# Performance work log

Hardware: AMD Instinct MI355X
Metric: run time of the kernel (lower is better)

Reference implementation:

```python
import jax, jax.numpy as jnp
import numpy as np

H, KV, D = 16, 4, 128
WIN = 512
EPS = 1e-6


def rms_norm(x, w):
    # x: [..., D]
    return x * jax.lax.rsqrt(jnp.mean(x * x, axis=-1, keepdims=True) + EPS) * w


def rotate_half(x):
    x1, x2 = jnp.split(x, 2, axis=-1)
    return jnp.concatenate([-x2, x1], axis=-1)


def setup_inputs() -> dict:
    key = jax.random.key(0)
    ks = jax.random.split(key, 8)
    B, L, hidden = 2, 2048, 2048
    x = jax.random.normal(ks[0], (B, L, hidden), jnp.float32)
    # realistic RoPE tables
    inv_freq = 1.0 / (10000.0 ** (np.arange(0, D, 2, dtype=np.float32) / D))
    t = np.arange(L, dtype=np.float32)
    freqs = np.outer(t, inv_freq)  # [L, D/2]
    emb = np.concatenate([freqs, freqs], axis=-1)  # [L, D]
    cos = jnp.asarray(np.cos(emb), jnp.float32)
    sin = jnp.asarray(np.sin(emb), jnp.float32)
    s = 0.02
    Wq = jax.random.normal(ks[1], (H * D, hidden), jnp.float32) * s
    Wk = jax.random.normal(ks[2], (KV * D, hidden), jnp.float32) * s
    Wv = jax.random.normal(ks[3], (KV * D, hidden), jnp.float32) * s
    Wo = jax.random.normal(ks[4], (hidden, H * D), jnp.float32) * s
    q_norm_w = jnp.ones((D,), jnp.float32)
    k_norm_w = jnp.ones((D,), jnp.float32)
    return {"x": x, "cos": cos, "sin": sin, "Wq": Wq, "Wk": Wk, "Wv": Wv,
            "Wo": Wo, "q_norm_w": q_norm_w, "k_norm_w": k_norm_w}


def reference(x, cos, sin, Wq, Wk, Wv, Wo, q_norm_w, k_norm_w):
    B, L, _ = x.shape
    # projections (torch Linear: y = x @ W.T)
    q = (x @ Wq.T).reshape(B, L, H, D)
    k = (x @ Wk.T).reshape(B, L, KV, D)
    v = (x @ Wv.T).reshape(B, L, KV, D)
    # QK RMSNorm, then [B, heads, L, D]
    q = jnp.transpose(rms_norm(q, q_norm_w), (0, 2, 1, 3))
    k = jnp.transpose(rms_norm(k, k_norm_w), (0, 2, 1, 3))
    v = jnp.transpose(v, (0, 2, 1, 3))
    # RoPE
    c = cos[None, None]  # [1,1,L,D]
    s = sin[None, None]
    q = q * c + rotate_half(q) * s
    k = k * c + rotate_half(k) * s
    # GQA repeat_interleave over head dim
    n_rep = H // KV
    k = jnp.repeat(k, n_rep, axis=1)
    v = jnp.repeat(v, n_rep, axis=1)
    # sliding-window additive bias [L, L]
    idx = jnp.arange(L)
    in_win = jnp.abs(idx[:, None] - idx[None, :]) <= WIN
    bias = jnp.where(in_win, 0.0, jnp.finfo(x.dtype).min).astype(x.dtype)
    # SDPA
    scale = 1.0 / jnp.sqrt(jnp.asarray(D, x.dtype))
    scores = jnp.einsum('bhqd,bhkd->bhqk', q, k) * scale + bias[None, None]
    attn = jax.nn.softmax(scores, axis=-1)
    out = jnp.einsum('bhqk,bhkd->bhqd', attn, v)  # [B,H,L,D]
    out = jnp.transpose(out, (0, 2, 1, 3)).reshape(B, L, H * D)
    return out @ Wo.T
```

## Files before the change

### kernel.cpp

```cpp
#include <hip/hip_runtime.h>
#include <hip/hip_bf16.h>


typedef unsigned short u16;
typedef unsigned int u32;
typedef __attribute__((ext_vector_type(8))) short bf16x8;
typedef __attribute__((ext_vector_type(4))) float f32x4;

#define AS1 __attribute__((address_space(1)))
#define AS3 __attribute__((address_space(3)))

__device__ __forceinline__ u16 f2b(float f) {
  union { float f; u32 u; } c; c.f = f;
  return (u16)((c.u + 0x8000u) >> 16);
}
__device__ __forceinline__ float b2f(u16 u) {
  union { u32 u; float f; } c; c.u = ((u32)u) << 16; return c.f;
}

__global__ __launch_bounds__(256) void cvt_all(const float* __restrict__ x,
                                               const float* __restrict__ wq,
                                               const float* __restrict__ wk,
                                               const float* __restrict__ wv,
                                               const float* __restrict__ wo,
                                               u16* __restrict__ xb,
                                               u16* __restrict__ wqkvb,
                                               u16* __restrict__ wob) {
  int blk = blockIdx.x;
  const float* s; u16* d; int off;
  if (blk < 8192)       { s = x;  d = xb;              off = blk * 1024; }
  else if (blk < 12288) { s = wq; d = wqkvb;           off = (blk - 8192) * 1024; }
  else if (blk < 13312) { s = wk; d = wqkvb + 4194304; off = (blk - 12288) * 1024; }
  else if (blk < 14336) { s = wv; d = wqkvb + 5242880; off = (blk - 13312) * 1024; }
  else                  { s = wo; d = wob;             off = (blk - 14336) * 1024; }
  int i = off + threadIdx.x * 4;
  float4 v = *(const float4*)(s + i);
  ushort4 o;
  o.x = f2b(v.x); o.y = f2b(v.y); o.z = f2b(v.z); o.w = f2b(v.w);
  *(ushort4*)(d + i) = o;
}

__global__ __launch_bounds__(256) void gemm_qkv(const u16* __restrict__ A,
                                                const u16* __restrict__ Bm,
                                                const float* __restrict__ cosT,
                                                const float* __restrict__ sinT,
                                                const float* __restrict__ qw,
                                                const float* __restrict__ kw,
                                                u16* __restrict__ qo,
                                                u16* __restrict__ ko,
                                                u16* __restrict__ vt) {
  constexpr int K = 2048;
  __shared__ u16 As[128][64];
  __shared__ u16 Bs[128][64];
  __shared__ float Rs[2][2][64];
  const int tid  = threadIdx.x;
  const int w    = tid >> 6, lane = tid & 63, quad = lane >> 4, l16 = lane & 15;
  const int wm   = w >> 1, wn = w & 1;
  const int m0   = blockIdx.y * 128;
  const int hh   = blockIdx.x;

  f32x4 zero = {0.f, 0.f, 0.f, 0.f};
  f32x4 acc[4][4];
#pragma unroll
  for (int i = 0; i < 4; i++)
#pragma unroll
    for (int j = 0; j < 4; j++) acc[i][j] = zero;

  const int srow = lane >> 3;
  const int swz8 = ((lane & 7) ^ (lane >> 3)) * 8;
  const int n0   = hh * 128;

  for (int k0 = 0; k0 < K; k0 += 64) {
#pragma unroll
    for (int p = 0; p < 4; ++p) {
      int row = p * 32 + w * 8 + srow;
      __builtin_amdgcn_global_load_lds(
          (const AS1 void*)(A + (size_t)(m0 + row) * K + k0 + swz8),
          (AS3 void*)((char*)&As[0][0] + p * 4096 + w * 1024), 16, 0, 0);
      __builtin_amdgcn_global_load_lds(
          (const AS1 void*)(Bm + (size_t)(n0 + row) * K + k0 + swz8),
          (AS3 void*)((char*)&Bs[0][0] + p * 4096 + w * 1024), 16, 0, 0);
    }
    __syncthreads();
#pragma unroll
    for (int kk = 0; kk < 64; kk += 32) {
      const int cs = ((kk >> 3) + quad) ^ (l16 & 7);
      bf16x8 af[4], bfr[4];
#pragma unroll
      for (int i = 0; i < 4; i++)
        af[i] = *(const bf16x8*)((const char*)&As[0][0] +
                                 (wm * 64 + i * 16 + l16) * 128 + cs * 16);
#pragma unroll
      for (int j = 0; j < 4; j++)
        bfr[j] = *(const bf16x8*)((const char*)&Bs[0][0] +
                                  (wn * 32 + (j & 1) * 16 + (j >> 1) * 64 + l16) * 128 + cs * 16);
#pragma unroll
      for (int i = 0; i < 4; i++)
#pragma unroll
        for (int j = 0; j < 4; j++)
          acc[i][j] = __builtin_amdgcn_mfma_f32_16x16x32_bf16(af[i], bfr[j], acc[i][j], 0, 0, 0);
    }
    __syncthreads();
  }

  const int bidx = m0 >> 11;
  const int lbase = (m0 & 2047) + wm * 64;

  if (hh < 20) {
    float ssq[4][4];
#pragma unroll
    for (int i = 0; i < 4; i++)
#pragma unroll
      for (int r = 0; r < 4; r++) {
        float s2 = acc[i][0][r] * acc[i][0][r] + acc[i][1][r] * acc[i][1][r] +
                   acc[i][2][r] * acc[i][2][r] + acc[i][3][r] * acc[i][3][r];
#pragma unroll
        for (int m = 1; m < 16; m <<= 1) s2 += __shfl_xor(s2, m, 64);
        ssq[i][r] = s2;
      }
    if (l16 == 0) {
#pragma unroll
      for (int i = 0; i < 4; i++)
#pragma unroll
        for (int r = 0; r < 4; r++)
          Rs[wm][wn][i * 16 + quad * 4 + r] = ssq[i][r];
    }
    __syncthreads();

    float inv[4][4];
#pragma unroll
    for (int i = 0; i < 4; i++)
#pragma unroll
      for (int r = 0; r < 4; r++) {
        int row64 = i * 16 + quad * 4 + r;
        float sum = Rs[wm][0][row64] + Rs[wm][1][row64];
        inv[i][r] = rsqrtf(sum * (1.0f / 128.0f) + 1e-6f);
      }

    const float* wt = hh < 16 ? qw : kw;
    const float qs_ = hh < 16 ? 0.08838834764831845f * 1.4426950408889634f : 1.0f;
    u16* dst; size_t hb;
    if (hh < 16) { dst = qo; hb = (size_t)(bidx * 16 + hh) * 2048 * 128; }
    else         { dst = ko; hb = (size_t)(bidx * 4 + (hh - 16)) * 2048 * 128; }

#pragma unroll
    for (int j = 0; j < 2; ++j) {
      const int d = wn * 32 + j * 16 + l16;
      const float wtd = wt[d], wtdp = wt[d + 64];
#pragma unroll
      for (int i = 0; i < 4; i++) {
#pragma unroll
        for (int r = 0; r < 4; r++) {
          int l = lbase + i * 16 + quad * 4 + r;
          float nv0 = acc[i][j][r]     * inv[i][r] * wtd;
          float nv1 = acc[i][j + 2][r] * inv[i][r] * wtdp;
          float c0 = cosT[l * 128 + d],      s0v = sinT[l * 128 + d];
          float c1 = cosT[l * 128 + d + 64], s1v = sinT[l * 128 + d + 64];
          float o0 = (nv0 * c0 - nv1 * s0v) * qs_;
          float o1 = (nv1 * c1 + nv0 * s1v) * qs_;
          dst[hb + (size_t)l * 128 + d]      = f2b(o0);
          dst[hb + (size_t)l * 128 + d + 64] = f2b(o1);
        }
      }
    }
  } else {
    const int kv = hh - 20;
    u16* dv = vt + (size_t)(bidx * 4 + kv) * 128 * 2048;
#pragma unroll
    for (int i = 0; i < 4; i++) {
      int l0 = lbase + i * 16 + quad * 4;
#pragma unroll
      for (int j = 0; j < 4; j++) {
        int d = wn * 32 + (j & 1) * 16 + (j >> 1) * 64 + l16;
        u16 p[4];
#pragma unroll
        for (int r = 0; r < 4; r++) p[r] = f2b(acc[i][j][r]);
        *(uint2*)(dv + (size_t)d * 2048 + l0) = *(uint2*)p;
      }
    }
  }
}

__global__ __launch_bounds__(256) void gemm_bt(const u16* __restrict__ A,
                                               const u16* __restrict__ Bm,
                                               float* __restrict__ C,
                                               int M, int N, int K) {
  __shared__ u16 As[128][64];
  __shared__ u16 Bs[128][64];
  const int tid  = threadIdx.x;
  const int w    = tid >> 6, lane = tid & 63, quad = lane >> 4, l16 = lane & 15;
  const int wm   = w >> 1, wn = w & 1;
  const int m0   = blockIdx.y * 128, n0 = blockIdx.x * 128;

  f32x4 zero = {0.f, 0.f, 0.f, 0.f};
  f32x4 acc[4][4];
#pragma unroll
  for (int i = 0; i < 4; i++)
#pragma unroll
    for (int j = 0; j < 4; j++) acc[i][j] = zero;

  const int srow = lane >> 3;
  const int swz8 = ((lane & 7) ^ (lane >> 3)) * 8;

  for (int k0 = 0; k0 < K; k0 += 64) {
#pragma unroll
    for (int p = 0; p < 4; ++p) {
      int row = p * 32 + w * 8 + srow;
      __builtin_amdgcn_global_load_lds(
          (const AS1 void*)(A + (size_t)(m0 + row) * K + k0 + swz8),
          (AS3 void*)((char*)&As[0][0] + p * 4096 + w * 1024), 16, 0, 0);
      __builtin_amdgcn_global_load_lds(
          (const AS1 void*)(Bm + (size_t)(n0 + row) * K + k0 + swz8),
          (AS3 void*)((char*)&Bs[0][0] + p * 4096 + w * 1024), 16, 0, 0);
    }
    __syncthreads();
#pragma unroll
    for (int kk = 0; kk < 64; kk += 32) {
      const int cs = ((kk >> 3) + quad) ^ (l16 & 7);
      bf16x8 af[4], bfr[4];
#pragma unroll
      for (int i = 0; i < 4; i++)
        af[i] = *(const bf16x8*)((const char*)&As[0][0] +
                                 (wm * 64 + i * 16 + l16) * 128 + cs * 16);
#pragma unroll
      for (int j = 0; j < 4; j++)
        bfr[j] = *(const bf16x8*)((const char*)&Bs[0][0] +
                                  (wn * 64 + j * 16 + l16) * 128 + cs * 16);
#pragma unroll
      for (int i = 0; i < 4; i++)
#pragma unroll
        for (int j = 0; j < 4; j++)
          acc[i][j] = __builtin_amdgcn_mfma_f32_16x16x32_bf16(af[i], bfr[j], acc[i][j], 0, 0, 0);
    }
    __syncthreads();
  }

#pragma unroll
  for (int i = 0; i < 4; i++) {
#pragma unroll
    for (int r = 0; r < 4; r++) {
      int gr = m0 + wm * 64 + i * 16 + quad * 4 + r;
#pragma unroll
      for (int j = 0; j < 4; j++) {
        int gc = n0 + wn * 64 + j * 16 + l16;
        C[(size_t)gr * N + gc] = acc[i][j][r];
      }
    }
  }
}

__global__ __launch_bounds__(512) void flash_swa(const u16* __restrict__ Q,
                                                 const u16* __restrict__ Kg,
                                                 const u16* __restrict__ VTg,
                                                 u16* __restrict__ Og) {
  constexpr int L = 2048, D = 128;
  __shared__ u16 Ks[2][64][128];
  __shared__ u16 Vt[2][128][64];
  __shared__ u16 Ps[8][32][72];

  const int flat = blockIdx.x;
  const int kvh  = flat & 3;
  const int b    = (flat >> 2) & 1;
  const int q0   = (flat >> 3) * 64;
  const int tid = threadIdx.x;
  const int w = tid >> 6, lane = tid & 63, quad = lane >> 4, l16 = lane & 15;
  const int hd = kvh * 4 + (w >> 1);
  const int qh = w & 1;

  const u16* Qb  = Q   + (size_t)(b * 16 + hd)  * L * D;
  const u16* Kb  = Kg  + (size_t)(b * 4 + kvh) * L * D;
  const u16* VTb = VTg + (size_t)(b * 4 + kvh) * D * L;

  bf16x8 qf[2][4];
#pragma unroll
  for (int qs = 0; qs < 2; ++qs) {
    int qr = q0 + qh * 32 + qs * 16 + l16;
#pragma unroll
    for (int ks = 0; ks < 4; ++ks)
      qf[qs][ks] = *(const bf16x8*)(Qb + (size_t)qr * D + ks * 32 + quad * 8);
  }
  const int qi0 = q0 + qh * 32 + l16;

  int kt0   = q0 > 512 ? q0 - 512 : 0;
  int ktend = q0 + 64 + 512; if (ktend > L) ktend = L;
  const int nt = (ktend - kt0) >> 6;

  const u16* srcK[2];
  const u16* srcV[2];
#pragma unroll
  for (int j = 0; j < 2; ++j) {
    int rk = w * 8 + j * 4 + quad;
    int ck = ((lane & 15) ^ (rk & 7)) * 8;
    srcK[j] = Kb + (size_t)(kt0 + rk) * D + ck;
    int rv = w * 16 + j * 8 + (lane >> 3);
    int cv = ((lane & 7) ^ ((lane >> 3) & 7)) * 8;
    srcV[j] = VTb + (size_t)rv * L + kt0 + cv;
  }

#define STAGE(bb) do {                                                        \
    char* kdst = (char*)&Ks[bb][0][0] + w * 2048;                             \
    char* vdst = (char*)&Vt[bb][0][0] + w * 2048;                             \
    _Pragma("unroll")                                                         \
    for (int j = 0; j < 2; ++j) {                                             \
      __builtin_amdgcn_global_load_lds((const AS1 void*)srcK[j],              \
          (AS3 void*)(kdst + j * 1024), 16, 0, 0);                            \
      srcK[j] += 64 * D;                                                      \
    }                                                                         \
    _Pragma("unroll")                                                         \
    for (int j = 0; j < 2; ++j) {                                             \
      __builtin_amdgcn_global_load_lds((const AS1 void*)srcV[j],              \
          (AS3 void*)(vdst + j * 1024), 16, 0, 0);                            \
      srcV[j] += 64;                                                          \
    }                                                                         \
  } while (0)

  f32x4 zero = {0.f, 0.f, 0.f, 0.f};
  f32x4 o[2][8];
#pragma unroll
  for (int qs = 0; qs < 2; ++qs)
#pragma unroll
    for (int i = 0; i < 8; i++) o[qs][i] = zero;
  float lrow[2] = {0.f, 0.f};

  STAGE(0);
  __syncthreads();
  int cur = 0;

  for (int t = 0; t < nt; ++t) {
    const int kt = kt0 + t * 64;
    if (t + 1 < nt) STAGE(cur ^ 1);

    const char* kbase = (const char*)&Ks[cur][0][0];
    const char* vbase = (const char*)&Vt[cur][0][0];

    f32x4 s[2][4];
#pragma unroll
    for (int qs = 0; qs < 2; ++qs)
#pragma unroll
      for (int ct = 0; ct < 4; ct++) s[qs][ct] = zero;
    __builtin_amdgcn_s_setprio(1);
#pragma unroll
    for (int ks = 0; ks < 4; ++ks) {
#pragma unroll
      for (int ct = 0; ct < 4; ++ct) {
        bf16x8 kf = *(const bf16x8*)(kbase + (ct * 16 + l16) * 256 +
                                     (((ks * 4 + quad) ^ (l16 & 7)) * 16));
        s[0][ct] = __builtin_amdgcn_mfma_f32_16x16x32_bf16(kf, qf[0][ks], s[0][ct], 0, 0, 0);
        s[1][ct] = __builtin_amdgcn_mfma_f32_16x16x32_bf16(kf, qf[1][ks], s[1][ct], 0, 0, 0);
      }
    }
    __builtin_amdgcn_s_setprio(0);

    bool need_mask = (kt + 448 < q0) || (kt > q0 + 448);
#pragma unroll
    for (int qs = 0; qs < 2; ++qs) {
      float psum = 0.f;
      u16* psw = &Ps[w][qs * 16 + l16][0];
#pragma unroll
      for (int ct = 0; ct < 4; ct++) {
        u16 ph[4];
#pragma unroll
        for (int r = 0; r < 4; r++) {
          float x = s[qs][ct][r];
          if (need_mask) {
            int ki = kt + ct * 16 + quad * 4 + r;
            int dd = (qi0 + qs * 16) - ki; if (dd < 0) dd = -dd;
            if (dd > 512) x = -__builtin_inff();
          }
          float p = exp2f(x);
          psum += p;
          ph[r] = f2b(p);
        }
        uint2 pk;
        pk.x = (u32)ph[0] | ((u32)ph[1] << 16);
        pk.y = (u32)ph[2] | ((u32)ph[3] << 16);
        *(uint2*)(psw + ct * 16 + quad * 4) = pk;
      }
      psum += __shfl_xor(psum, 16, 64);
      psum += __shfl_xor(psum, 32, 64);
      lrow[qs] += psum;
    }

    bf16x8 pf[2][2];
#pragma unroll
    for (int qs = 0; qs < 2; ++qs) {
#pragma unroll
      for (int ks2 = 0; ks2 < 2; ++ks2)
        pf[qs][ks2] = *(const bf16x8*)(&Ps[w][qs * 16 + l16][ks2 * 32 + quad * 8]);
    }
    __builtin_amdgcn_s_setprio(1);
#pragma unroll
    for (int dt = 0; dt < 8; ++dt) {
#pragma unroll
      for (int ks2 = 0; ks2 < 2; ++ks2) {
        bf16x8 vf = *(const bf16x8*)(vbase + (dt * 16 + l16) * 128 +
                                     (((ks2 * 4 + quad) ^ (l16 & 7)) * 16));
        o[0][dt] = __builtin_amdgcn_mfma_f32_16x16x32_bf16(pf[0][ks2], vf, o[0][dt], 0, 0, 0);
        o[1][dt] = __builtin_amdgcn_mfma_f32_16x16x32_bf16(pf[1][ks2], vf, o[1][dt], 0, 0, 0);
      }
    }
    __builtin_amdgcn_s_setprio(0);

    __syncthreads();
    cur ^= 1;
  }
#undef STAGE

#pragma unroll
  for (int qs = 0; qs < 2; ++qs) {
#pragma unroll
    for (int r = 0; r < 4; r++) {
      float lv  = __shfl(lrow[qs], (lane & 48) + quad * 4 + r, 64);
      float inv = 1.0f / lv;
      int qr = q0 + qh * 32 + qs * 16 + quad * 4 + r;
      size_t base = ((size_t)(b * L + qr)) * 2048 + hd * 128;
#pragma unroll
      for (int dt = 0; dt < 8; dt++)
        Og[base + dt * 16 + l16] = f2b(o[qs][dt][r] * inv);
    }
  }
}

extern "C" void kernel_launch(void* const* d_in, const int* in_sizes, int n_in,
                              void* d_out, int out_size, void* d_ws, size_t ws_size,
                              hipStream_t stream) {
  const float* x    = (const float*)d_in[0];
  const float* cosT = (const float*)d_in[1];
  const float* sinT = (const float*)d_in[2];
  const float* Wq   = (const float*)d_in[3];
  const float* Wk   = (const float*)d_in[4];
  const float* Wv   = (const float*)d_in[5];
  const float* Wo   = (const float*)d_in[6];
  const float* qw   = (const float*)d_in[7];
  const float* kw   = (const float*)d_in[8];

  char* ws = (char*)d_ws;
  u16* x_bf    = (u16*)(ws + 0);
  u16* wqkv_bf = (u16*)(ws + 16777216);
  u16* wo_bf   = (u16*)(ws + 29360128);
  u16* vt_bf   = (u16*)(ws + 37748736);
  u16* q_bf    = (u16*)(ws + 62914560);
  u16* k_bf    = (u16*)(ws + 79691776);
  u16* attn_bf = x_bf;

  cvt_all<<<18432, 256, 0, stream>>>(x, Wq, Wk, Wv, Wo, x_bf, wqkv_bf, wo_bf);
  gemm_qkv<<<dim3(24, 32), 256, 0, stream>>>(x_bf, wqkv_bf, cosT, sinT, qw, kw,
                                             q_bf, k_bf, vt_bf);
  flash_swa<<<dim3(256, 1, 1), 512, 0, stream>>>(q_bf, k_bf, vt_bf, attn_bf);
  gemm_bt<<<dim3(16, 32), 256, 0, stream>>>(attn_bf, wo_bf, (float*)d_out,
                                            4096, 2048, 2048);
}
```

Baseline: 309.3 us.

## Write V row-major from QKV GEMM and transpose it in a separate kernel

The QKV GEMM epilogue now writes V in row-major [B, L, 512] layout instead of scattering 8-byte strided stores into a transposed buffer. A new LDS-tiled transpose kernel then builds the [B*KV, D, L] layout that the attention kernel expects. The Q/K norm epilogue is also restructured to compute inverse RMS on the fly and keep fewer values live in registers. In exchange the change adds an extra kernel launch and an extra round trip of V through memory, and the row-major V stores are now 2-byte scalar writes.

```diff
diff --git a/kernel.cpp b/kernel.cpp
--- a/kernel.cpp
+++ b/kernel.cpp
@@ -48,7 +48,7 @@
                                                 const float* __restrict__ kw,
                                                 u16* __restrict__ qo,
                                                 u16* __restrict__ ko,
-                                                u16* __restrict__ vt) {
+                                                u16* __restrict__ vb) {
   constexpr int K = 2048;
   __shared__ u16 As[128][64];
   __shared__ u16 Bs[128][64];
@@ -107,35 +107,18 @@
   const int lbase = (m0 & 2047) + wm * 64;
 
   if (hh < 20) {
-    float ssq[4][4];
-#pragma unroll
-    for (int i = 0; i < 4; i++)
+#pragma unroll
+    for (int i = 0; i < 4; i++) {
 #pragma unroll
       for (int r = 0; r < 4; r++) {
         float s2 = acc[i][0][r] * acc[i][0][r] + acc[i][1][r] * acc[i][1][r] +
                    acc[i][2][r] * acc[i][2][r] + acc[i][3][r] * acc[i][3][r];
 #pragma unroll
         for (int m = 1; m < 16; m <<= 1) s2 += __shfl_xor(s2, m, 64);
-        ssq[i][r] = s2;
-      }
-    if (l16 == 0) {
-#pragma unroll
-      for (int i = 0; i < 4; i++)
-#pragma unroll
-        for (int r = 0; r < 4; r++)
-          Rs[wm][wn][i * 16 + quad * 4 + r] = ssq[i][r];
-    }
-    __syncthreads();
-
-    float inv[4][4];
-#pragma unroll
-    for (int i = 0; i < 4; i++)
-#pragma unroll
-      for (int r = 0; r < 4; r++) {
-        int row64 = i * 16 + quad * 4 + r;
-        float sum = Rs[wm][0][row64] + Rs[wm][1][row64];
-        inv[i][r] = rsqrtf(sum * (1.0f / 128.0f) + 1e-6f);
-      }
+        if (l16 == 0) Rs[wm][wn][i * 16 + quad * 4 + r] = s2;
+      }
+    }
+    __syncthreads();
 
     const float* wt = hh < 16 ? qw : kw;
     const float qs_ = hh < 16 ? 0.08838834764831845f * 1.4426950408889634f : 1.0f;
@@ -143,21 +126,26 @@
     if (hh < 16) { dst = qo; hb = (size_t)(bidx * 16 + hh) * 2048 * 128; }
     else         { dst = ko; hb = (size_t)(bidx * 4 + (hh - 16)) * 2048 * 128; }
 
-#pragma unroll
-    for (int j = 0; j < 2; ++j) {
-      const int d = wn * 32 + j * 16 + l16;
-      const float wtd = wt[d], wtdp = wt[d + 64];
-#pragma unroll
-      for (int i = 0; i < 4; i++) {
-#pragma unroll
-        for (int r = 0; r < 4; r++) {
-          int l = lbase + i * 16 + quad * 4 + r;
-          float nv0 = acc[i][j][r]     * inv[i][r] * wtd;
-          float nv1 = acc[i][j + 2][r] * inv[i][r] * wtdp;
-          float c0 = cosT[l * 128 + d],      s0v = sinT[l * 128 + d];
-          float c1 = cosT[l * 128 + d + 64], s1v = sinT[l * 128 + d + 64];
-          float o0 = (nv0 * c0 - nv1 * s0v) * qs_;
-          float o1 = (nv1 * c1 + nv0 * s1v) * qs_;
+    const int d0 = wn * 32 + l16;
+    const float wt00 = wt[d0],      wt01 = wt[d0 + 64];
+    const float wt10 = wt[d0 + 16], wt11 = wt[d0 + 80];
+
+#pragma unroll
+    for (int i = 0; i < 4; i++) {
+#pragma unroll
+      for (int r = 0; r < 4; r++) {
+        int row64 = i * 16 + quad * 4 + r;
+        float inv = rsqrtf((Rs[wm][0][row64] + Rs[wm][1][row64]) * (1.0f / 128.0f) + 1e-6f);
+        int l = lbase + i * 16 + quad * 4 + r;
+        const float* cl = cosT + l * 128;
+        const float* sl = sinT + l * 128;
+#pragma unroll
+        for (int j = 0; j < 2; ++j) {
+          int d = d0 + j * 16;
+          float nv0 = acc[i][j][r]     * inv * (j ? wt10 : wt00);
+          float nv1 = acc[i][j + 2][r] * inv * (j ? wt11 : wt01);
+          float o0 = (nv0 * cl[d]      - nv1 * sl[d])      * qs_;
+          float o1 = (nv1 * cl[d + 64] + nv0 * sl[d + 64]) * qs_;
           dst[hb + (size_t)l * 128 + d]      = f2b(o0);
           dst[hb + (size_t)l * 128 + d + 64] = f2b(o1);
         }
@@ -165,19 +153,42 @@
     }
   } else {
     const int kv = hh - 20;
-    u16* dv = vt + (size_t)(bidx * 4 + kv) * 128 * 2048;
+    u16* dv = vb + (size_t)bidx * 2048 * 512;
 #pragma unroll
     for (int i = 0; i < 4; i++) {
-      int l0 = lbase + i * 16 + quad * 4;
-#pragma unroll
-      for (int j = 0; j < 4; j++) {
-        int d = wn * 32 + (j & 1) * 16 + (j >> 1) * 64 + l16;
-        u16 p[4];
-#pragma unroll
-        for (int r = 0; r < 4; r++) p[r] = f2b(acc[i][j][r]);
-        *(uint2*)(dv + (size_t)d * 2048 + l0) = *(uint2*)p;
-      }
-    }
+#pragma unroll
+      for (int r = 0; r < 4; r++) {
+        int gr = lbase + i * 16 + quad * 4 + r;
+#pragma unroll
+        for (int j = 0; j < 4; j++) {
+          int gc = kv * 128 + wn * 32 + (j & 1) * 16 + (j >> 1) * 64 + l16;
+          dv[(size_t)gr * 512 + gc] = f2b(acc[i][j][r]);
+        }
+      }
+    }
+  }
+}
+
+__global__ __launch_bounds__(256) void transpose_v(const u16* __restrict__ vb,
+                                                   u16* __restrict__ dst) {
+  __shared__ u16 T[64][72];
+  const int lt = blockIdx.x, dt = blockIdx.y, bh = blockIdx.z;
+  const int b = bh >> 2, kv = bh & 3;
+  const u16* s = vb + ((size_t)(b * 2048 + lt * 64)) * 512 + kv * 128 + dt * 64;
+  u16*       d = dst + (size_t)bh * 128 * 2048 + (size_t)dt * 64 * 2048 + lt * 64;
+  const int t = threadIdx.x;
+  const int row = t >> 3, c8 = (t & 7) * 8;
+#pragma unroll
+  for (int p = 0; p < 2; ++p)
+    *(uint4*)&T[p * 32 + row][c8] = *(const uint4*)(s + (size_t)(p * 32 + row) * 512 + c8);
+  __syncthreads();
+#pragma unroll
+  for (int p = 0; p < 2; ++p) {
+    int dr = p * 32 + row;
+    u16 o[8];
+#pragma unroll
+    for (int j = 0; j < 8; ++j) o[j] = T[c8 + j][dr];
+    *(uint4*)(d + (size_t)dr * 2048 + c8) = *(uint4*)o;
   }
 }
 
@@ -438,14 +449,16 @@
   u16* x_bf    = (u16*)(ws + 0);
   u16* wqkv_bf = (u16*)(ws + 16777216);
   u16* wo_bf   = (u16*)(ws + 29360128);
-  u16* vt_bf   = (u16*)(ws + 37748736);
+  u16* vbuf    = (u16*)(ws + 37748736);
+  u16* vt_bf   = (u16*)(ws + 41943040);
   u16* q_bf    = (u16*)(ws + 62914560);
   u16* k_bf    = (u16*)(ws + 79691776);
   u16* attn_bf = x_bf;
 
   cvt_all<<<18432, 256, 0, stream>>>(x, Wq, Wk, Wv, Wo, x_bf, wqkv_bf, wo_bf);
   gemm_qkv<<<dim3(24, 32), 256, 0, stream>>>(x_bf, wqkv_bf, cosT, sinT, qw, kw,
-                                             q_bf, k_bf, vt_bf);
+                                             q_bf, k_bf, vbuf);
+  transpose_v<<<dim3(32, 2, 8), 256, 0, stream>>>(vbuf, vt_bf);
   flash_swa<<<dim3(256, 1, 1), 512, 0, stream>>>(q_bf, k_bf, vt_bf, attn_bf);
   gemm_bt<<<dim3(16, 32), 256, 0, stream>>>(attn_bf, wo_bf, (float*)d_out,
                                             4096, 2048, 2048);
```

Result: no change. 312.4 us (+1.0%).
